# Performance work log

Measured on AMD Instinct MI355X. Metric: run time of the kernel, lower is better.

## Reference

```python
import jax, jax.numpy as jnp
import numpy as np

H = 64  # hidden size

def _lstm_last_h(x, W_ih, W_hh, b_ih, b_hh):
    # x: [B, T]; PyTorch LSTM gate order: i, f, g, o (each H wide in 4H axis)
    B, T = x.shape
    # input_size == 1, so x @ W_ih.T == x[..., None] * W_ih[:, 0]
    xproj = x[:, :, None] * W_ih[:, 0][None, None, :] + (b_ih + b_hh)  # [B, T, 4H]
    xproj_t = jnp.swapaxes(xproj, 0, 1)  # [T, B, 4H] for scan over time

    def step(carry, xp_t):
        h, c = carry
        gates = xp_t + h @ W_hh.T  # [B, 4H]
        i = jax.nn.sigmoid(gates[:, 0 * H:1 * H])
        f = jax.nn.sigmoid(gates[:, 1 * H:2 * H])
        g = jnp.tanh(gates[:, 2 * H:3 * H])
        o = jax.nn.sigmoid(gates[:, 3 * H:4 * H])
        c = f * c + i * g
        h = o * jnp.tanh(c)
        return (h, c), None

    h0 = jnp.zeros((B, H), x.dtype)
    c0 = jnp.zeros((B, H), x.dtype)
    (h_last, _), _ = jax.lax.scan(step, (h0, c0), xproj_t)
    return h_last  # [B, H] == lstm_out[:, -1, :]


def setup_inputs() -> dict:
    key = jax.random.key(0)
    ks = jax.random.split(key, 7)
    B, T = 2048, 512
    s_ih = 1.0 / np.sqrt(H)
    return {
        "x": jax.random.normal(ks[0], (B, T), jnp.float32),
        "W_ih": jax.random.uniform(ks[1], (4 * H, 1), jnp.float32, -s_ih, s_ih),
        "W_hh": jax.random.uniform(ks[2], (4 * H, H), jnp.float32, -s_ih, s_ih),
        "b_ih": jax.random.uniform(ks[3], (4 * H,), jnp.float32, -s_ih, s_ih),
        "b_hh": jax.random.uniform(ks[4], (4 * H,), jnp.float32, -s_ih, s_ih),
        "W_d": jax.random.uniform(ks[5], (1, H), jnp.float32, -s_ih, s_ih),
        "b_d": jax.random.uniform(ks[6], (1,), jnp.float32, -s_ih, s_ih),
    }


def reference(x, W_ih, W_hh, b_ih, b_hh, W_d, b_d):
    h_last = _lstm_last_h(x, W_ih, W_hh, b_ih, b_hh)  # [B, H]
    out = h_last @ W_d.T + b_d  # [B, 1]
    return out[:, 0]  # squeeze(1) -> [B]
```

## Files before the change

kernel.cpp:

```cpp
#include <hip/hip_runtime.h>

#define TLEN 512
#define HID  64

typedef _Float16 half8 __attribute__((ext_vector_type(8)));
typedef float    f32x4 __attribute__((ext_vector_type(4)));

__device__ __forceinline__ float rcp_fast(float x) { return __builtin_amdgcn_rcpf(x); }
__device__ __forceinline__ float sigmoid_fast(float x) { return rcp_fast(1.0f + __expf(-x)); }
__device__ __forceinline__ float tanh_fast(float x) { return 1.0f - 2.0f * rcp_fast(__expf(2.0f * x) + 1.0f); }

__global__ __launch_bounds__(256) __attribute__((amdgpu_waves_per_eu(2, 2)))
void lstm_mfma4(const float* __restrict__ x,
                const float* __restrict__ W_ih,
                const float* __restrict__ W_hh,
                const float* __restrict__ b_ih,
                const float* __restrict__ b_hh,
                const float* __restrict__ W_d,
                const float* __restrict__ b_d,
                float* __restrict__ out) {
    __shared__ __align__(16) float    xs[4][516];
    __shared__ __align__(16) _Float16 hbuf[2][4][72];

    const int tid = threadIdx.x;
    const int L   = tid & 63;
    const int w   = tid >> 6;
    const int r0  = blockIdx.x * 4;

    for (int i = tid; i < 4 * 128; i += 256) {
        const int r = i >> 7, t4 = (i & 127) * 4;
        *(float4*)&xs[r][t4] = *(const float4*)&x[(size_t)(r0 + r) * TLEN + t4];
    }
    for (int i = tid; i < 2 * 4 * 72; i += 256)
        ((_Float16*)hbuf)[i] = (_Float16)0.0f;

    half8 af[4][2];
    {
        const int m = L & 15;
        const int g = m & 3;
        const int kb = (L >> 4) * 8;
#pragma unroll
        for (int tt = 0; tt < 4; ++tt) {
            const int uu = 16 * w + 4 * tt + (m >> 2);
            const float* row = &W_hh[(size_t)(g * HID + uu) * HID];
#pragma unroll
            for (int q = 0; q < 2; ++q) {
                const float* p = row + 32 * q + kb;
                half8 hf;
#pragma unroll
                for (int i = 0; i < 8; ++i) hf[i] = (_Float16)p[i];
                af[tt][q] = hf;
            }
        }
    }

    const int b   = L & 3;
    const int sel = (L >> 2) & 3;
    const int u   = 16 * w + 4 * sel + (L >> 4);

    float wih[4], bias[4];
#pragma unroll
    for (int g = 0; g < 4; ++g) {
        wih[g]  = W_ih[g * HID + u];
        bias[g] = b_ih[g * HID + u] + b_hh[g * HID + u];
    }

    const float* xrow = &xs[b][0];
    const int koff = (L >> 4) * 8;
    const _Float16* h0r = &hbuf[0][b][0];
    _Float16*       h0w = &hbuf[0][b][0];
    const _Float16* h1r = &hbuf[1][b][0];
    _Float16*       h1w = &hbuf[1][b][0];
    const f32x4 zero = {0.0f, 0.0f, 0.0f, 0.0f};
    float cst = 0.0f;

    __syncthreads();

    auto step = [&](const _Float16* hin, _Float16* hout, float xt) {
        half8 b0 = *(const half8*)(hin + koff);
        half8 b1 = *(const half8*)(hin + koff + 32);

        f32x4 d0 = __builtin_amdgcn_mfma_f32_16x16x32_f16(af[0][0], b0, zero, 0, 0, 0);
        f32x4 d1 = __builtin_amdgcn_mfma_f32_16x16x32_f16(af[1][0], b0, zero, 0, 0, 0);
        f32x4 d2 = __builtin_amdgcn_mfma_f32_16x16x32_f16(af[2][0], b0, zero, 0, 0, 0);
        f32x4 d3 = __builtin_amdgcn_mfma_f32_16x16x32_f16(af[3][0], b0, zero, 0, 0, 0);
        d0 = __builtin_amdgcn_mfma_f32_16x16x32_f16(af[0][1], b1, d0, 0, 0, 0);
        d1 = __builtin_amdgcn_mfma_f32_16x16x32_f16(af[1][1], b1, d1, 0, 0, 0);
        d2 = __builtin_amdgcn_mfma_f32_16x16x32_f16(af[2][1], b1, d2, 0, 0, 0);
        d3 = __builtin_amdgcn_mfma_f32_16x16x32_f16(af[3][1], b1, d3, 0, 0, 0);

        const f32x4 d = sel == 0 ? d0 : (sel == 1 ? d1 : (sel == 2 ? d2 : d3));

        const float ai  = d[0] + fmaf(xt, wih[0], bias[0]);
        const float afv = d[1] + fmaf(xt, wih[1], bias[1]);
        const float ag  = d[2] + fmaf(xt, wih[2], bias[2]);
        const float ao  = d[3] + fmaf(xt, wih[3], bias[3]);
        const float gi = sigmoid_fast(ai);
        const float gf = sigmoid_fast(afv);
        const float gg = tanh_fast(ag);
        const float go = sigmoid_fast(ao);
        cst = fmaf(gf, cst, gi * gg);
        const float hv = go * tanh_fast(cst);
        hout[u] = (_Float16)hv;
    };

    for (int t = 0; t < TLEN; t += 2) {
        step(h0r, h1w, xrow[t]);
        __syncthreads();
        step(h1r, h0w, xrow[t + 1]);
        __syncthreads();
    }

    float pv = (float)hbuf[0][w][L] * W_d[L];
#pragma unroll
    for (int off = 32; off > 0; off >>= 1)
        pv += __shfl_xor(pv, off, 64);
    if (L == 0)
        out[r0 + w] = pv + b_d[0];
}

extern "C" void kernel_launch(void* const* d_in, const int* in_sizes, int n_in,
                              void* d_out, int out_size, void* d_ws, size_t ws_size,
                              hipStream_t stream) {
    const float* x    = (const float*)d_in[0];
    const float* W_ih = (const float*)d_in[1];
    const float* W_hh = (const float*)d_in[2];
    const float* b_ih = (const float*)d_in[3];
    const float* b_hh = (const float*)d_in[4];
    const float* W_d  = (const float*)d_in[5];
    const float* b_d  = (const float*)d_in[6];
    float* out = (float*)d_out;

    dim3 grid(512);
    dim3 block(256);
    lstm_mfma4<<<grid, block, 0, stream>>>(x, W_ih, W_hh, b_ih, b_hh, W_d, b_d, out);
}
```

Baseline: 235.3 us.

## Split LSTM gate units across eight waves and fold exp scaling into weights

Doubles the block to eight waves, so each wave owns 8 hidden units and issues 4 MFMAs per step instead of 8. This shortens the serial per-step matrix chain on the recurrent critical path. Gate activations now call exp2 directly, with the log2(e) and sign factors pre-multiplied into the input weights and biases, which removes per-step multiplies. The trade-off is that barriers now synchronize twice as many waves per step, and half the lanes do redundant duplicate work.

```diff
diff --git a/kernel.cpp b/kernel.cpp
--- a/kernel.cpp
+++ b/kernel.cpp
@@ -7,11 +7,16 @@
 typedef float    f32x4 __attribute__((ext_vector_type(4)));
 
 __device__ __forceinline__ float rcp_fast(float x) { return __builtin_amdgcn_rcpf(x); }
-__device__ __forceinline__ float sigmoid_fast(float x) { return rcp_fast(1.0f + __expf(-x)); }
-__device__ __forceinline__ float tanh_fast(float x) { return 1.0f - 2.0f * rcp_fast(__expf(2.0f * x) + 1.0f); }
+__device__ __forceinline__ float exp2_fast(float x) {
+#if __has_builtin(__builtin_amdgcn_exp2f)
+    return __builtin_amdgcn_exp2f(x);
+#else
+    float r; asm("v_exp_f32 %0, %1" : "=v"(r) : "v"(x)); return r;
+#endif
+}
 
-__global__ __launch_bounds__(256) __attribute__((amdgpu_waves_per_eu(2, 2)))
-void lstm_mfma4(const float* __restrict__ x,
+__global__ __launch_bounds__(512) __attribute__((amdgpu_waves_per_eu(4, 4)))
+void lstm_mfma5(const float* __restrict__ x,
                 const float* __restrict__ W_ih,
                 const float* __restrict__ W_hh,
                 const float* __restrict__ b_ih,
@@ -27,21 +32,21 @@
     const int w   = tid >> 6;
     const int r0  = blockIdx.x * 4;
 
-    for (int i = tid; i < 4 * 128; i += 256) {
+    for (int i = tid; i < 4 * 128; i += 512) {
         const int r = i >> 7, t4 = (i & 127) * 4;
         *(float4*)&xs[r][t4] = *(const float4*)&x[(size_t)(r0 + r) * TLEN + t4];
     }
-    for (int i = tid; i < 2 * 4 * 72; i += 256)
+    for (int i = tid; i < 2 * 4 * 72; i += 512)
         ((_Float16*)hbuf)[i] = (_Float16)0.0f;
 
-    half8 af[4][2];
+    half8 af[2][2];
     {
         const int m = L & 15;
         const int g = m & 3;
         const int kb = (L >> 4) * 8;
 #pragma unroll
-        for (int tt = 0; tt < 4; ++tt) {
-            const int uu = 16 * w + 4 * tt + (m >> 2);
+        for (int tt = 0; tt < 2; ++tt) {
+            const int uu = 8 * w + 4 * tt + (m >> 2);
             const float* row = &W_hh[(size_t)(g * HID + uu) * HID];
 #pragma unroll
             for (int q = 0; q < 2; ++q) {
@@ -54,15 +59,19 @@
         }
     }
 
-    const int b   = L & 3;
-    const int sel = (L >> 2) & 3;
-    const int u   = 16 * w + 4 * sel + (L >> 4);
+    const int c   = L & 15;
+    const int b   = c & 3;
+    const int sel = (c >> 2) & 1;
+    const int u   = 8 * w + 4 * sel + (L >> 4);
 
-    float wih[4], bias[4];
+    const float K = 1.44269504f;
+    float wih[4], bias[4], dscl[4];
 #pragma unroll
     for (int g = 0; g < 4; ++g) {
-        wih[g]  = W_ih[g * HID + u];
-        bias[g] = b_ih[g * HID + u] + b_hh[g * HID + u];
+        const float s = (g == 2) ? 2.0f * K : -K;
+        wih[g]  = s * W_ih[g * HID + u];
+        bias[g] = s * (b_ih[g * HID + u] + b_hh[g * HID + u]);
+        dscl[g] = s;
     }
 
     const float* xrow = &xs[b][0];
@@ -82,25 +91,22 @@
 
         f32x4 d0 = __builtin_amdgcn_mfma_f32_16x16x32_f16(af[0][0], b0, zero, 0, 0, 0);
         f32x4 d1 = __builtin_amdgcn_mfma_f32_16x16x32_f16(af[1][0], b0, zero, 0, 0, 0);
-        f32x4 d2 = __builtin_amdgcn_mfma_f32_16x16x32_f16(af[2][0], b0, zero, 0, 0, 0);
-        f32x4 d3 = __builtin_amdgcn_mfma_f32_16x16x32_f16(af[3][0], b0, zero, 0, 0, 0);
         d0 = __builtin_amdgcn_mfma_f32_16x16x32_f16(af[0][1], b1, d0, 0, 0, 0);
         d1 = __builtin_amdgcn_mfma_f32_16x16x32_f16(af[1][1], b1, d1, 0, 0, 0);
-        d2 = __builtin_amdgcn_mfma_f32_16x16x32_f16(af[2][1], b1, d2, 0, 0, 0);
-        d3 = __builtin_amdgcn_mfma_f32_16x16x32_f16(af[3][1], b1, d3, 0, 0, 0);
 
-        const f32x4 d = sel == 0 ? d0 : (sel == 1 ? d1 : (sel == 2 ? d2 : d3));
+        const f32x4 d = sel ? d1 : d0;
 
-        const float ai  = d[0] + fmaf(xt, wih[0], bias[0]);
-        const float afv = d[1] + fmaf(xt, wih[1], bias[1]);
-        const float ag  = d[2] + fmaf(xt, wih[2], bias[2]);
-        const float ao  = d[3] + fmaf(xt, wih[3], bias[3]);
-        const float gi = sigmoid_fast(ai);
-        const float gf = sigmoid_fast(afv);
-        const float gg = tanh_fast(ag);
-        const float go = sigmoid_fast(ao);
+        const float ei = exp2_fast(fmaf(d[0], dscl[0], fmaf(xt, wih[0], bias[0])));
+        const float ef = exp2_fast(fmaf(d[1], dscl[1], fmaf(xt, wih[1], bias[1])));
+        const float eg = exp2_fast(fmaf(d[2], dscl[2], fmaf(xt, wih[2], bias[2])));
+        const float eo = exp2_fast(fmaf(d[3], dscl[3], fmaf(xt, wih[3], bias[3])));
+        const float gi = rcp_fast(1.0f + ei);
+        const float gf = rcp_fast(1.0f + ef);
+        const float gg = fmaf(-2.0f, rcp_fast(1.0f + eg), 1.0f);
+        const float go = rcp_fast(1.0f + eo);
         cst = fmaf(gf, cst, gi * gg);
-        const float hv = go * tanh_fast(cst);
+        const float tc = fmaf(-2.0f, rcp_fast(1.0f + exp2_fast(2.0f * K * cst)), 1.0f);
+        const float hv = go * tc;
         hout[u] = (_Float16)hv;
     };
 
@@ -111,12 +117,14 @@
         __syncthreads();
     }
 
-    float pv = (float)hbuf[0][w][L] * W_d[L];
+    if (w < 4) {
+        float pv = (float)hbuf[0][w][L] * W_d[L];
 #pragma unroll
-    for (int off = 32; off > 0; off >>= 1)
-        pv += __shfl_xor(pv, off, 64);
-    if (L == 0)
-        out[r0 + w] = pv + b_d[0];
+        for (int off = 32; off > 0; off >>= 1)
+            pv += __shfl_xor(pv, off, 64);
+        if (L == 0)
+            out[r0 + w] = pv + b_d[0];
+    }
 }
 
 extern "C" void kernel_launch(void* const* d_in, const int* in_sizes, int n_in,
@@ -132,6 +140,6 @@
     float* out = (float*)d_out;
 
     dim3 grid(512);
-    dim3 block(256);
-    lstm_mfma4<<<grid, block, 0, stream>>>(x, W_ih, W_hh, b_ih, b_hh, W_d, b_d, out);
+    dim3 block(512);
+    lstm_mfma5<<<grid, block, 0, stream>>>(x, W_ih, W_hh, b_ih, b_hh, W_d, b_d, out);
 }
```

Result: slower. 282.9 us (+20.2%).
